# Kernel tuning notes

Hardware: AMD Instinct MI355X
Metric: run time of the kernel (lower is better)

Reference implementation:

```python
import jax, jax.numpy as jnp
import numpy as np

WS = 7          # window_size
NUM_HEADS = 8
EPS = 1e-5


def _layernorm(x, g, b):
    m = jnp.mean(x, axis=-1, keepdims=True)
    v = jnp.var(x, axis=-1, keepdims=True)
    return (x - m) * jax.lax.rsqrt(v + EPS) * g + b


def _window_attention(win, w_qkv, b_qkv, w_proj, b_proj):
    B_, L, C = win.shape
    h = NUM_HEADS
    d = C // h
    scale = d ** -0.5
    qkv = win @ w_qkv.T + b_qkv                      # (B_, L, 3C)
    qkv = qkv.reshape(B_, L, 3, h, d).transpose(2, 0, 3, 1, 4)  # (3, B_, h, L, d)
    q, k, v = qkv[0], qkv[1], qkv[2]
    attn = jnp.einsum('bhld,bhmd->bhlm', q, k) * scale
    attn = jax.nn.softmax(attn, axis=-1)
    out = jnp.einsum('bhlm,bhmd->bhld', attn, v)     # (B_, h, L, d)
    out = out.transpose(0, 2, 1, 3).reshape(B_, L, C)
    return out @ w_proj.T + b_proj


def _forward(x, H, W, g1, b1, w_qkv, b_qkv, w_proj, b_proj, g2, b2,
             w_fc1, b_fc1, w_fc2, b_fc2):
    N, L, C = x.shape
    shortcut = x
    y = _layernorm(x, g1, b1).reshape(N, H, W, C)
    pad_h = (WS - H % WS) % WS
    pad_w = (WS - W % WS) % WS
    y = jnp.pad(y, ((0, 0), (0, pad_h), (0, pad_w), (0, 0)))
    Hp, Wp = H + pad_h, W + pad_w
    # window partition: (N, Hp/WS, WS, Wp/WS, WS, C) -> (N*nW, WS*WS, C)
    y = y.reshape(N, Hp // WS, WS, Wp // WS, WS, C).transpose(0, 1, 3, 2, 4, 5)
    windows = y.reshape(-1, WS * WS, C)
    attn_windows = _window_attention(windows, w_qkv, b_qkv, w_proj, b_proj)
    # window reverse
    y = attn_windows.reshape(N, Hp // WS, Wp // WS, WS, WS, C)
    y = y.transpose(0, 1, 3, 2, 4, 5).reshape(N, Hp, Wp, C)[:, :H, :W, :]
    y = y.reshape(N, H * W, C)
    x = shortcut + y
    # MLP: Linear -> GELU (erf, torch default) -> Linear
    z = _layernorm(x, g2, b2)
    z = jax.nn.gelu(z @ w_fc1.T + b_fc1, approximate=False) @ w_fc2.T + b_fc2
    return x + z


def setup_inputs() -> dict:
    key = jax.random.key(0)
    ks = jax.random.split(key, 8)
    N, H, W, C = 8, 112, 112, 256
    hidden = 4 * C
    s = 0.02
    return {
        'x': jax.random.normal(ks[0], (N, H * W, C), jnp.float32),
        'H': H,
        'W': W,
        'g1': jnp.ones((C,), jnp.float32),
        'b1': jnp.zeros((C,), jnp.float32),
        'w_qkv': jax.random.normal(ks[1], (3 * C, C), jnp.float32) * s,
        'b_qkv': jnp.zeros((3 * C,), jnp.float32),
        'w_proj': jax.random.normal(ks[2], (C, C), jnp.float32) * s,
        'b_proj': jnp.zeros((C,), jnp.float32),
        'g2': jnp.ones((C,), jnp.float32),
        'b2': jnp.zeros((C,), jnp.float32),
        'w_fc1': jax.random.normal(ks[3], (hidden, C), jnp.float32) * s,
        'b_fc1': jnp.zeros((hidden,), jnp.float32),
        'w_fc2': jax.random.normal(ks[4], (C, hidden), jnp.float32) * s,
        'b_fc2': jnp.zeros((C,), jnp.float32),
    }


def reference(x, H, W, g1, b1, w_qkv, b_qkv, w_proj, b_proj, g2, b2,
              w_fc1, b_fc1, w_fc2, b_fc2):
    return _forward(x, H, W, g1, b1, w_qkv, b_qkv, w_proj, b_proj,
                    g2, b2, w_fc1, b_fc1, w_fc2, b_fc2)
```

## Files before the change

### kernel.cpp

```cpp
#include <hip/hip_runtime.h>
#include <hip/hip_bf16.h>
#include <cstdint>
#include <cstddef>


typedef __bf16 bf16x8 __attribute__((ext_vector_type(8)));
typedef float f32x4 __attribute__((ext_vector_type(4)));

__device__ __forceinline__ unsigned short f2bf(float f){
    union{float f;uint32_t u;}c;c.f=f;uint32_t u=c.u;u+=0x7fffu+((u>>16)&1u);return (unsigned short)(u>>16);}
__device__ __forceinline__ float gelu_f(float x){ return 0.5f*x*(1.0f+erff(x*0.70710678118654752f)); }
__device__ __forceinline__ int swz(int row,int g){ return (g & ~7) | ((g ^ row) & 7); }

__global__ __launch_bounds__(256) void conv_k(
    const float* __restrict__ src, unsigned short* __restrict__ dst, int n4)
{
    int i = blockIdx.x * 256 + threadIdx.x;
    if (i >= n4) return;
    float4 v = *(const float4*)(src + (size_t)i * 4);
    uint2 o;
    o.x = (uint32_t)f2bf(v.x) | ((uint32_t)f2bf(v.y) << 16);
    o.y = (uint32_t)f2bf(v.z) | ((uint32_t)f2bf(v.w) << 16);
    *(uint2*)(dst + (size_t)i * 4) = o;
}

__global__ __launch_bounds__(1024, 4) void attn_half_k(
    const float* __restrict__ x, const float* __restrict__ g1, const float* __restrict__ b1,
    const unsigned short* __restrict__ Wqkv, const float* __restrict__ bqkv,
    const unsigned short* __restrict__ Wproj, const float* __restrict__ bproj,
    float* __restrict__ out)
{
    __shared__ __align__(16) unsigned short yb[64 * 256];
    __shared__ __align__(16) unsigned short qkb[64 * 512];
    __shared__ __align__(16) unsigned short vtb[256 * 64];
    const int t = threadIdx.x, lane = t & 63, w = t >> 6;
    const int quad = lane >> 4, l16 = lane & 15;
    const int widx = blockIdx.x;
    const int img = widx >> 8, wi = widx & 255;
    const int wy = wi >> 4, wx = wi & 15;
    const size_t ibase = (size_t)img * 12544;

    for (int tok = w; tok < 49; tok += 16) {
        int r = tok / 7, c = tok - r * 7;
        size_t gtok = ibase + (size_t)(wy * 7 + r) * 112 + (wx * 7 + c);
        float4 v = *(const float4*)(x + gtok * 256 + lane * 4);
        float s = v.x + v.y + v.z + v.w;
        float q = v.x*v.x + v.y*v.y + v.z*v.z + v.w*v.w;
        #pragma unroll
        for (int o = 32; o > 0; o >>= 1) { s += __shfl_xor(s, o); q += __shfl_xor(q, o); }
        float mean = s * (1.f/256.f), var = q * (1.f/256.f) - mean * mean;
        float inv = rsqrtf(var + 1e-5f);
        float4 gv = *(const float4*)(g1 + lane * 4);
        float4 bv = *(const float4*)(b1 + lane * 4);
        uint2 pk;
        pk.x = (uint32_t)f2bf((v.x-mean)*inv*gv.x+bv.x) | ((uint32_t)f2bf((v.y-mean)*inv*gv.y+bv.y) << 16);
        pk.y = (uint32_t)f2bf((v.z-mean)*inv*gv.z+bv.z) | ((uint32_t)f2bf((v.w-mean)*inv*gv.w+bv.w) << 16);
        *(uint2*)&yb[tok*256 + swz(tok, lane >> 1)*8 + (lane & 1)*4] = pk;
    }
    {
        uint2 z2; z2.x = 0u; z2.y = 0u;
        for (int i = t; i < 960; i += 1024) {
            int row = 49 + (i >> 6), c4 = (i & 63) * 4;
            *(uint2*)&yb[row*256 + c4] = z2;
        }
    }
    __syncthreads();

    {
        const int n0 = w * 48;
        f32x4 acc[4][3] = {};
        #pragma unroll
        for (int ks = 0; ks < 8; ++ks) {
            bf16x8 af[4], bfr[3];
            #pragma unroll
            for (int mt = 0; mt < 4; ++mt) {
                int m = mt * 16 + l16;
                af[mt] = *(const bf16x8*)&yb[m*256 + swz(m, ks*4 + quad)*8];
            }
            #pragma unroll
            for (int nt = 0; nt < 3; ++nt) {
                int n = n0 + nt * 16 + l16;
                bfr[nt] = *(const bf16x8*)(Wqkv + (size_t)n*256 + ks*32 + quad*8);
            }
            #pragma unroll
            for (int mt = 0; mt < 4; ++mt)
                #pragma unroll
                for (int nt = 0; nt < 3; ++nt)
                    acc[mt][nt] = __builtin_amdgcn_mfma_f32_16x16x32_bf16(
                        af[mt], bfr[nt], acc[mt][nt], 0, 0, 0);
        }
        #pragma unroll
        for (int mt = 0; mt < 4; ++mt)
            #pragma unroll
            for (int nt = 0; nt < 3; ++nt) {
                int col = n0 + nt * 16 + l16;
                float bb = bqkv[col];
                #pragma unroll
                for (int r = 0; r < 4; ++r) {
                    int row = mt * 16 + quad * 4 + r;
                    unsigned short val = f2bf(acc[mt][nt][r] + bb);
                    if (col < 512)
                        qkb[row*512 + swz(row, col >> 3)*8 + (col & 7)] = val;
                    else
                        vtb[(col - 512)*64 + swz(col - 512, row >> 3)*8 + (row & 7)] = val;
                }
            }
    }
    __syncthreads();

    {
        const float scale = 0.17677669529663687f;
        const int h = w & 7, half = w >> 3;
        unsigned short* pbuf = qkb + w * 1280;

        bf16x8 aq[2], bk[4];
        #pragma unroll
        for (int mtl = 0; mtl < 2; ++mtl) {
            int m = half*32 + mtl*16 + l16;
            aq[mtl] = *(const bf16x8*)&qkb[m*512 + swz(m, h*4 + quad)*8];
        }
        #pragma unroll
        for (int nt = 0; nt < 4; ++nt) {
            int n = nt * 16 + l16;
            bk[nt] = *(const bf16x8*)&qkb[n*512 + swz(n, 32 + h*4 + quad)*8];
        }
        __syncthreads();

        f32x4 s[2][4] = {};
        #pragma unroll
        for (int mtl = 0; mtl < 2; ++mtl)
            #pragma unroll
            for (int nt = 0; nt < 4; ++nt)
                s[mtl][nt] = __builtin_amdgcn_mfma_f32_16x16x32_bf16(
                    aq[mtl], bk[nt], s[mtl][nt], 0, 0, 0);

        uint32_t pk01[2][4], pk23[2][4];
        #pragma unroll
        for (int mtl = 0; mtl < 2; ++mtl)
            #pragma unroll
            for (int r = 0; r < 4; ++r) {
                float v0 = s[mtl][0][r];
                float v1 = s[mtl][1][r];
                float v2 = s[mtl][2][r];
                float v3 = (l16 == 0) ? s[mtl][3][r] : -1e30f;
                float mxv = fmaxf(fmaxf(v0, v1), fmaxf(v2, v3));
                #pragma unroll
                for (int off = 8; off > 0; off >>= 1) mxv = fmaxf(mxv, __shfl_xor(mxv, off));
                float p0 = __expf((v0 - mxv) * scale);
                float p1 = __expf((v1 - mxv) * scale);
                float p2 = __expf((v2 - mxv) * scale);
                float p3 = __expf((v3 - mxv) * scale);
                float ssum = p0 + p1 + p2 + p3;
                #pragma unroll
                for (int off = 8; off > 0; off >>= 1) ssum += __shfl_xor(ssum, off);
                float inv = 1.f / ssum;
                pk01[mtl][r] = (uint32_t)f2bf(p0*inv) | ((uint32_t)f2bf(p1*inv) << 16);
                pk23[mtl][r] = (uint32_t)f2bf(p2*inv) | ((uint32_t)f2bf(p3*inv) << 16);
            }

        f32x4 o[2][2] = {};
        #pragma unroll
        for (int kst = 0; kst < 2; ++kst) {
            #pragma unroll
            for (int mtl = 0; mtl < 2; ++mtl)
                #pragma unroll
                for (int r = 0; r < 4; ++r) {
                    int lr = mtl*16 + quad*4 + r;
                    uint32_t pw = kst ? pk23[mtl][r] : pk01[mtl][r];
                    pbuf[lr*40 + l16]      = (unsigned short)(pw & 0xffffu);
                    pbuf[lr*40 + 16 + l16] = (unsigned short)(pw >> 16);
                }
            bf16x8 ap[2], bv[2];
            #pragma unroll
            for (int mtl = 0; mtl < 2; ++mtl) {
                int m = mtl * 16 + l16;
                ap[mtl] = *(const bf16x8*)&pbuf[m*40 + quad*8];
            }
            #pragma unroll
            for (int nt = 0; nt < 2; ++nt) {
                int c = h*32 + nt*16 + l16;
                bv[nt] = *(const bf16x8*)&vtb[c*64 + swz(c, kst*4 + quad)*8];
            }
            #pragma unroll
            for (int mtl = 0; mtl < 2; ++mtl)
                #pragma unroll
                for (int nt = 0; nt < 2; ++nt)
                    o[mtl][nt] = __builtin_amdgcn_mfma_f32_16x16x32_bf16(
                        ap[mtl], bv[nt], o[mtl][nt], 0, 0, 0);
        }
        __syncthreads();

        #pragma unroll
        for (int mtl = 0; mtl < 2; ++mtl)
            #pragma unroll
            for (int nt = 0; nt < 2; ++nt)
                #pragma unroll
                for (int r = 0; r < 4; ++r) {
                    int row = half*32 + mtl*16 + quad*4 + r;
                    int ch = h*32 + nt*16 + l16;
                    float val = (row < 49) ? o[mtl][nt][r] : 0.f;
                    qkb[row*512 + swz(row, ch >> 3)*8 + (ch & 7)] = f2bf(val);
                }
    }
    __syncthreads();

    {
        const int n0 = w * 16;
        f32x4 acc[4];
        #pragma unroll
        for (int mt = 0; mt < 4; ++mt) acc[mt] = (f32x4){0.f,0.f,0.f,0.f};
        #pragma unroll
        for (int ks = 0; ks < 8; ++ks) {
            bf16x8 af[4], bfr;
            #pragma unroll
            for (int mt = 0; mt < 4; ++mt) {
                int m = mt * 16 + l16;
                af[mt] = *(const bf16x8*)&qkb[m*512 + swz(m, ks*4 + quad)*8];
            }
            {
                int n = n0 + l16;
                bfr = *(const bf16x8*)(Wproj + (size_t)n*256 + ks*32 + quad*8);
            }
            #pragma unroll
            for (int mt = 0; mt < 4; ++mt)
                acc[mt] = __builtin_amdgcn_mfma_f32_16x16x32_bf16(
                    af[mt], bfr, acc[mt], 0, 0, 0);
        }
        #pragma unroll
        for (int mt = 0; mt < 4; ++mt)
            #pragma unroll
            for (int r = 0; r < 4; ++r) {
                int row = mt * 16 + quad * 4 + r;
                if (row < 49) {
                    int rr = row / 7, cc = row - rr * 7;
                    size_t gtok = ibase + (size_t)(wy * 7 + rr) * 112 + (wx * 7 + cc);
                    int col = n0 + l16;
                    out[gtok * 256 + col] = acc[mt][r] + bproj[col] + x[gtok * 256 + col];
                }
            }
    }
}

__global__ __launch_bounds__(512, 4) void mlp_half_k(
    const float* __restrict__ g2, const float* __restrict__ b2,
    const unsigned short* __restrict__ W1, const float* __restrict__ bf1,
    const unsigned short* __restrict__ W2, const float* __restrict__ bf2,
    float* __restrict__ out)
{
    __shared__ __align__(16) unsigned short zb[64 * 256];
    __shared__ __align__(16) unsigned short hb[64 * 256];
    const int t = threadIdx.x, lane = t & 63, w = t >> 6;
    const int quad = lane >> 4, l16 = lane & 15;
    const size_t m0 = (size_t)blockIdx.x * 64;

    for (int tok = w; tok < 64; tok += 8) {
        size_t row = m0 + tok;
        float4 v = *(const float4*)&out[row*256 + lane*4];
        float s = v.x+v.y+v.z+v.w, q = v.x*v.x+v.y*v.y+v.z*v.z+v.w*v.w;
        #pragma unroll
        for (int o = 32; o > 0; o >>= 1) { s += __shfl_xor(s, o); q += __shfl_xor(q, o); }
        float mean = s*(1.f/256.f), var = q*(1.f/256.f) - mean*mean;
        float inv = rsqrtf(var + 1e-5f);
        float4 gv = *(const float4*)(g2 + lane*4);
        float4 bv = *(const float4*)(b2 + lane*4);
        uint2 pk;
        pk.x = (uint32_t)f2bf((v.x-mean)*inv*gv.x+bv.x) | ((uint32_t)f2bf((v.y-mean)*inv*gv.y+bv.y) << 16);
        pk.y = (uint32_t)f2bf((v.z-mean)*inv*gv.z+bv.z) | ((uint32_t)f2bf((v.w-mean)*inv*gv.w+bv.w) << 16);
        *(uint2*)&zb[tok*256 + swz(tok, lane >> 1)*8 + (lane & 1)*4] = pk;
    }
    __syncthreads();

    f32x4 acc2[4][2] = {};
    for (int c = 0; c < 4; ++c) {
        const int hc0 = c * 256;
        f32x4 acc1[4][2] = {};
        #pragma unroll
        for (int ks = 0; ks < 8; ++ks) {
            bf16x8 af[4], bfr[2];
            #pragma unroll
            for (int mt = 0; mt < 4; ++mt) {
                int m = mt * 16 + l16;
                af[mt] = *(const bf16x8*)&zb[m*256 + swz(m, ks*4 + quad)*8];
            }
            #pragma unroll
            for (int nt = 0; nt < 2; ++nt) {
                int n = hc0 + w * 32 + nt * 16 + l16;
                bfr[nt] = *(const bf16x8*)(W1 + (size_t)n*256 + ks*32 + quad*8);
            }
            #pragma unroll
            for (int mt = 0; mt < 4; ++mt)
                #pragma unroll
                for (int nt = 0; nt < 2; ++nt)
                    acc1[mt][nt] = __builtin_amdgcn_mfma_f32_16x16x32_bf16(
                        af[mt], bfr[nt], acc1[mt][nt], 0, 0, 0);
        }
        __syncthreads();
        #pragma unroll
        for (int mt = 0; mt < 4; ++mt)
            #pragma unroll
            for (int nt = 0; nt < 2; ++nt) {
                int lc = w * 32 + nt * 16 + l16;
                float bb = bf1[hc0 + lc];
                #pragma unroll
                for (int r = 0; r < 4; ++r) {
                    int row = mt * 16 + quad * 4 + r;
                    hb[row*256 + swz(row, lc >> 3)*8 + (lc & 7)] =
                        f2bf(gelu_f(acc1[mt][nt][r] + bb));
                }
            }
        __syncthreads();
        #pragma unroll
        for (int ks = 0; ks < 8; ++ks) {
            bf16x8 af[4], bfr[2];
            #pragma unroll
            for (int mt = 0; mt < 4; ++mt) {
                int m = mt * 16 + l16;
                af[mt] = *(const bf16x8*)&hb[m*256 + swz(m, ks*4 + quad)*8];
            }
            #pragma unroll
            for (int nt = 0; nt < 2; ++nt) {
                int n = w * 32 + nt * 16 + l16;
                bfr[nt] = *(const bf16x8*)(W2 + (size_t)n*1024 + hc0 + ks*32 + quad*8);
            }
            #pragma unroll
            for (int mt = 0; mt < 4; ++mt)
                #pragma unroll
                for (int nt = 0; nt < 2; ++nt)
                    acc2[mt][nt] = __builtin_amdgcn_mfma_f32_16x16x32_bf16(
                        af[mt], bfr[nt], acc2[mt][nt], 0, 0, 0);
        }
    }
    #pragma unroll
    for (int mt = 0; mt < 4; ++mt)
        #pragma unroll
        for (int nt = 0; nt < 2; ++nt) {
            int col = w * 32 + nt * 16 + l16;
            float bb = bf2[col];
            #pragma unroll
            for (int r = 0; r < 4; ++r) {
                size_t row = m0 + mt * 16 + quad * 4 + r;
                out[row*256 + col] = acc2[mt][nt][r] + bb + out[row*256 + col];
            }
        }
}

extern "C" void kernel_launch(void* const* d_in, const int* in_sizes, int n_in,
                              void* d_out, int out_size, void* d_ws, size_t ws_size,
                              hipStream_t stream)
{
    const float* x      = (const float*)d_in[0];
    const float* g1     = (const float*)d_in[3];
    const float* b1     = (const float*)d_in[4];
    const float* w_qkv  = (const float*)d_in[5];
    const float* b_qkv  = (const float*)d_in[6];
    const float* w_proj = (const float*)d_in[7];
    const float* b_proj = (const float*)d_in[8];
    const float* g2     = (const float*)d_in[9];
    const float* b2     = (const float*)d_in[10];
    const float* w_fc1  = (const float*)d_in[11];
    const float* b_fc1  = (const float*)d_in[12];
    const float* w_fc2  = (const float*)d_in[13];
    const float* b_fc2  = (const float*)d_in[14];
    float* out = (float*)d_out;

    unsigned short* cWqkv  = (unsigned short*)d_ws;
    unsigned short* cWproj = cWqkv  + 196608;
    unsigned short* cWfc1  = cWproj + 65536;
    unsigned short* cWfc2  = cWfc1  + 262144;

    conv_k<<<192, 256, 0, stream>>>(w_qkv,  cWqkv,  49152);
    conv_k<<<64,  256, 0, stream>>>(w_proj, cWproj, 16384);
    conv_k<<<256, 256, 0, stream>>>(w_fc1,  cWfc1,  65536);
    conv_k<<<256, 256, 0, stream>>>(w_fc2,  cWfc2,  65536);

    attn_half_k<<<2048, 1024, 0, stream>>>(x, g1, b1, cWqkv, b_qkv, cWproj, b_proj, out);
    mlp_half_k<<<1568, 512, 0, stream>>>(g2, b2, cWfc1, b_fc1, cWfc2, b_fc2, out);
}
```

Baseline: 716.0 us.

## Stage epilogues through LDS for coalesced float4 stores and widen MLP block

Both kernels now write their GEMM outputs to shared memory and then do residual adds with coalesced float4 global loads and stores, replacing scattered scalar global writes. The MLP kernel doubles its threads to 1024 so each wave computes 16 columns instead of 32, and pads LDS row strides (QKP, MP, SP) to cut bank conflicts. LayerNorm token loads are batched into registers so several global loads are in flight before the reductions run. The changes add extra barriers and more LDS per block, and per-wave register pressure shifts.

```diff
diff --git a/kernel.cpp b/kernel.cpp
--- a/kernel.cpp
+++ b/kernel.cpp
@@ -24,6 +24,7 @@
     *(uint2*)(dst + (size_t)i * 4) = o;
 }
 
+#define QKP 520
 __global__ __launch_bounds__(1024, 4) void attn_half_k(
     const float* __restrict__ x, const float* __restrict__ g1, const float* __restrict__ b1,
     const unsigned short* __restrict__ Wqkv, const float* __restrict__ bqkv,
@@ -31,7 +32,7 @@
     float* __restrict__ out)
 {
     __shared__ __align__(16) unsigned short yb[64 * 256];
-    __shared__ __align__(16) unsigned short qkb[64 * 512];
+    __shared__ __align__(16) unsigned short qkb[64 * QKP];
     __shared__ __align__(16) unsigned short vtb[256 * 64];
     const int t = threadIdx.x, lane = t & 63, w = t >> 6;
     const int quad = lane >> 4, l16 = lane & 15;
@@ -40,22 +41,36 @@
     const int wy = wi >> 4, wx = wi & 15;
     const size_t ibase = (size_t)img * 12544;
 
-    for (int tok = w; tok < 49; tok += 16) {
-        int r = tok / 7, c = tok - r * 7;
-        size_t gtok = ibase + (size_t)(wy * 7 + r) * 112 + (wx * 7 + c);
-        float4 v = *(const float4*)(x + gtok * 256 + lane * 4);
-        float s = v.x + v.y + v.z + v.w;
-        float q = v.x*v.x + v.y*v.y + v.z*v.z + v.w*v.w;
-        #pragma unroll
-        for (int o = 32; o > 0; o >>= 1) { s += __shfl_xor(s, o); q += __shfl_xor(q, o); }
-        float mean = s * (1.f/256.f), var = q * (1.f/256.f) - mean * mean;
-        float inv = rsqrtf(var + 1e-5f);
+    {
+        float4 xv[4];
+        #pragma unroll
+        for (int i = 0; i < 4; ++i) {
+            int tok = w + i * 16;
+            if (tok < 49) {
+                int r = tok / 7, c = tok - r * 7;
+                size_t gtok = ibase + (size_t)(wy * 7 + r) * 112 + (wx * 7 + c);
+                xv[i] = *(const float4*)(x + gtok * 256 + lane * 4);
+            }
+        }
         float4 gv = *(const float4*)(g1 + lane * 4);
         float4 bv = *(const float4*)(b1 + lane * 4);
-        uint2 pk;
-        pk.x = (uint32_t)f2bf((v.x-mean)*inv*gv.x+bv.x) | ((uint32_t)f2bf((v.y-mean)*inv*gv.y+bv.y) << 16);
-        pk.y = (uint32_t)f2bf((v.z-mean)*inv*gv.z+bv.z) | ((uint32_t)f2bf((v.w-mean)*inv*gv.w+bv.w) << 16);
-        *(uint2*)&yb[tok*256 + swz(tok, lane >> 1)*8 + (lane & 1)*4] = pk;
+        #pragma unroll
+        for (int i = 0; i < 4; ++i) {
+            int tok = w + i * 16;
+            if (tok < 49) {
+                float4 v = xv[i];
+                float s = v.x + v.y + v.z + v.w;
+                float q = v.x*v.x + v.y*v.y + v.z*v.z + v.w*v.w;
+                #pragma unroll
+                for (int o = 32; o > 0; o >>= 1) { s += __shfl_xor(s, o); q += __shfl_xor(q, o); }
+                float mean = s * (1.f/256.f), var = q * (1.f/256.f) - mean * mean;
+                float inv = rsqrtf(var + 1e-5f);
+                uint2 pk;
+                pk.x = (uint32_t)f2bf((v.x-mean)*inv*gv.x+bv.x) | ((uint32_t)f2bf((v.y-mean)*inv*gv.y+bv.y) << 16);
+                pk.y = (uint32_t)f2bf((v.z-mean)*inv*gv.z+bv.z) | ((uint32_t)f2bf((v.w-mean)*inv*gv.w+bv.w) << 16);
+                *(uint2*)&yb[tok*256 + swz(tok, lane >> 1)*8 + (lane & 1)*4] = pk;
+            }
+        }
     }
     {
         uint2 z2; z2.x = 0u; z2.y = 0u;
@@ -100,7 +115,7 @@
                     int row = mt * 16 + quad * 4 + r;
                     unsigned short val = f2bf(acc[mt][nt][r] + bb);
                     if (col < 512)
-                        qkb[row*512 + swz(row, col >> 3)*8 + (col & 7)] = val;
+                        qkb[row*QKP + swz(row, col >> 3)*8 + (col & 7)] = val;
                     else
                         vtb[(col - 512)*64 + swz(col - 512, row >> 3)*8 + (row & 7)] = val;
                 }
@@ -117,12 +132,12 @@
         #pragma unroll
         for (int mtl = 0; mtl < 2; ++mtl) {
             int m = half*32 + mtl*16 + l16;
-            aq[mtl] = *(const bf16x8*)&qkb[m*512 + swz(m, h*4 + quad)*8];
+            aq[mtl] = *(const bf16x8*)&qkb[m*QKP + swz(m, h*4 + quad)*8];
         }
         #pragma unroll
         for (int nt = 0; nt < 4; ++nt) {
             int n = nt * 16 + l16;
-            bk[nt] = *(const bf16x8*)&qkb[n*512 + swz(n, 32 + h*4 + quad)*8];
+            bk[nt] = *(const bf16x8*)&qkb[n*QKP + swz(n, 32 + h*4 + quad)*8];
         }
         __syncthreads();
 
@@ -199,7 +214,7 @@
                     int row = half*32 + mtl*16 + quad*4 + r;
                     int ch = h*32 + nt*16 + l16;
                     float val = (row < 49) ? o[mtl][nt][r] : 0.f;
-                    qkb[row*512 + swz(row, ch >> 3)*8 + (ch & 7)] = f2bf(val);
+                    qkb[row*QKP + swz(row, ch >> 3)*8 + (ch & 7)] = f2bf(val);
                 }
     }
     __syncthreads();
@@ -215,7 +230,7 @@
             #pragma unroll
             for (int mt = 0; mt < 4; ++mt) {
                 int m = mt * 16 + l16;
-                af[mt] = *(const bf16x8*)&qkb[m*512 + swz(m, ks*4 + quad)*8];
+                af[mt] = *(const bf16x8*)&qkb[m*QKP + swz(m, ks*4 + quad)*8];
             }
             {
                 int n = n0 + l16;
@@ -226,122 +241,158 @@
                 acc[mt] = __builtin_amdgcn_mfma_f32_16x16x32_bf16(
                     af[mt], bfr, acc[mt], 0, 0, 0);
         }
-        #pragma unroll
-        for (int mt = 0; mt < 4; ++mt)
-            #pragma unroll
-            for (int r = 0; r < 4; ++r) {
-                int row = mt * 16 + quad * 4 + r;
+        float* sb = (float*)yb;
+        float4 bp = *(const float4*)(bproj + lane * 4);
+        #pragma unroll
+        for (int batch = 0; batch < 2; ++batch) {
+            #pragma unroll
+            for (int mt = 2*batch; mt < 2*batch + 2; ++mt)
+                #pragma unroll
+                for (int r = 0; r < 4; ++r) {
+                    int row = mt * 16 + quad * 4 + r;
+                    sb[(row - batch*32)*256 + n0 + l16] = acc[mt][r];
+                }
+            __syncthreads();
+            #pragma unroll
+            for (int i = 0; i < 2; ++i) {
+                int row = batch*32 + w*2 + i;
                 if (row < 49) {
                     int rr = row / 7, cc = row - rr * 7;
                     size_t gtok = ibase + (size_t)(wy * 7 + rr) * 112 + (wx * 7 + cc);
-                    int col = n0 + l16;
-                    out[gtok * 256 + col] = acc[mt][r] + bproj[col] + x[gtok * 256 + col];
-                }
-            }
+                    float4 xr = *(const float4*)(x + gtok * 256 + lane * 4);
+                    float4 sv = *(const float4*)&sb[(row - batch*32)*256 + lane * 4];
+                    float4 o4;
+                    o4.x = sv.x + bp.x + xr.x;
+                    o4.y = sv.y + bp.y + xr.y;
+                    o4.z = sv.z + bp.z + xr.z;
+                    o4.w = sv.w + bp.w + xr.w;
+                    *(float4*)&out[gtok * 256 + lane * 4] = o4;
+                }
+            }
+            __syncthreads();
+        }
     }
 }
 
-__global__ __launch_bounds__(512, 4) void mlp_half_k(
+#define MP 264
+#define SP 260
+__global__ __launch_bounds__(1024, 8) void mlp_half_k(
     const float* __restrict__ g2, const float* __restrict__ b2,
     const unsigned short* __restrict__ W1, const float* __restrict__ bf1,
     const unsigned short* __restrict__ W2, const float* __restrict__ bf2,
     float* __restrict__ out)
 {
-    __shared__ __align__(16) unsigned short zb[64 * 256];
-    __shared__ __align__(16) unsigned short hb[64 * 256];
+    __shared__ __align__(16) unsigned short smem[2 * 64 * MP];
+    unsigned short* zb = smem;
+    unsigned short* hb = smem + 64 * MP;
     const int t = threadIdx.x, lane = t & 63, w = t >> 6;
     const int quad = lane >> 4, l16 = lane & 15;
     const size_t m0 = (size_t)blockIdx.x * 64;
 
-    for (int tok = w; tok < 64; tok += 8) {
-        size_t row = m0 + tok;
-        float4 v = *(const float4*)&out[row*256 + lane*4];
-        float s = v.x+v.y+v.z+v.w, q = v.x*v.x+v.y*v.y+v.z*v.z+v.w*v.w;
-        #pragma unroll
-        for (int o = 32; o > 0; o >>= 1) { s += __shfl_xor(s, o); q += __shfl_xor(q, o); }
-        float mean = s*(1.f/256.f), var = q*(1.f/256.f) - mean*mean;
-        float inv = rsqrtf(var + 1e-5f);
+    {
+        float4 xv[4];
+        #pragma unroll
+        for (int i = 0; i < 4; ++i) {
+            size_t row = m0 + w + i * 16;
+            xv[i] = *(const float4*)&out[row*256 + lane*4];
+        }
         float4 gv = *(const float4*)(g2 + lane*4);
         float4 bv = *(const float4*)(b2 + lane*4);
-        uint2 pk;
-        pk.x = (uint32_t)f2bf((v.x-mean)*inv*gv.x+bv.x) | ((uint32_t)f2bf((v.y-mean)*inv*gv.y+bv.y) << 16);
-        pk.y = (uint32_t)f2bf((v.z-mean)*inv*gv.z+bv.z) | ((uint32_t)f2bf((v.w-mean)*inv*gv.w+bv.w) << 16);
-        *(uint2*)&zb[tok*256 + swz(tok, lane >> 1)*8 + (lane & 1)*4] = pk;
+        #pragma unroll
+        for (int i = 0; i < 4; ++i) {
+            int tok = w + i * 16;
+            float4 v = xv[i];
+            float s = v.x+v.y+v.z+v.w, q = v.x*v.x+v.y*v.y+v.z*v.z+v.w*v.w;
+            #pragma unroll
+            for (int o = 32; o > 0; o >>= 1) { s += __shfl_xor(s, o); q += __shfl_xor(q, o); }
+            float mean = s*(1.f/256.f), var = q*(1.f/256.f) - mean*mean;
+            float inv = rsqrtf(var + 1e-5f);
+            uint2 pk;
+            pk.x = (uint32_t)f2bf((v.x-mean)*inv*gv.x+bv.x) | ((uint32_t)f2bf((v.y-mean)*inv*gv.y+bv.y) << 16);
+            pk.y = (uint32_t)f2bf((v.z-mean)*inv*gv.z+bv.z) | ((uint32_t)f2bf((v.w-mean)*inv*gv.w+bv.w) << 16);
+            *(uint2*)&zb[tok*MP + swz(tok, lane >> 1)*8 + (lane & 1)*4] = pk;
+        }
     }
     __syncthreads();
 
-    f32x4 acc2[4][2] = {};
+    f32x4 acc2[4] = {};
     for (int c = 0; c < 4; ++c) {
         const int hc0 = c * 256;
-        f32x4 acc1[4][2] = {};
+        f32x4 acc1[4] = {};
         #pragma unroll
         for (int ks = 0; ks < 8; ++ks) {
-            bf16x8 af[4], bfr[2];
+            bf16x8 af[4], bfr;
             #pragma unroll
             for (int mt = 0; mt < 4; ++mt) {
                 int m = mt * 16 + l16;
-                af[mt] = *(const bf16x8*)&zb[m*256 + swz(m, ks*4 + quad)*8];
-            }
-            #pragma unroll
-            for (int nt = 0; nt < 2; ++nt) {
-                int n = hc0 + w * 32 + nt * 16 + l16;
-                bfr[nt] = *(const bf16x8*)(W1 + (size_t)n*256 + ks*32 + quad*8);
+                af[mt] = *(const bf16x8*)&zb[m*MP + swz(m, ks*4 + quad)*8];
+            }
+            {
+                int n = hc0 + w * 16 + l16;
+                bfr = *(const bf16x8*)(W1 + (size_t)n*256 + ks*32 + quad*8);
             }
             #pragma unroll
             for (int mt = 0; mt < 4; ++mt)
-                #pragma unroll
-                for (int nt = 0; nt < 2; ++nt)
-                    acc1[mt][nt] = __builtin_amdgcn_mfma_f32_16x16x32_bf16(
-                        af[mt], bfr[nt], acc1[mt][nt], 0, 0, 0);
+                acc1[mt] = __builtin_amdgcn_mfma_f32_16x16x32_bf16(
+                    af[mt], bfr, acc1[mt], 0, 0, 0);
         }
         __syncthreads();
-        #pragma unroll
-        for (int mt = 0; mt < 4; ++mt)
-            #pragma unroll
-            for (int nt = 0; nt < 2; ++nt) {
-                int lc = w * 32 + nt * 16 + l16;
-                float bb = bf1[hc0 + lc];
+        {
+            int lc = w * 16 + l16;
+            float bb = bf1[hc0 + lc];
+            #pragma unroll
+            for (int mt = 0; mt < 4; ++mt)
                 #pragma unroll
                 for (int r = 0; r < 4; ++r) {
                     int row = mt * 16 + quad * 4 + r;
-                    hb[row*256 + swz(row, lc >> 3)*8 + (lc & 7)] =
-                        f2bf(gelu_f(acc1[mt][nt][r] + bb));
-                }
-            }
+                    hb[row*MP + swz(row, lc >> 3)*8 + (lc & 7)] =
+                        f2bf(gelu_f(acc1[mt][r] + bb));
+                }
+        }
         __syncthreads();
         #pragma unroll
         for (int ks = 0; ks < 8; ++ks) {
-            bf16x8 af[4], bfr[2];
+            bf16x8 af[4], bfr;
             #pragma unroll
             for (int mt = 0; mt < 4; ++mt) {
                 int m = mt * 16 + l16;
-                af[mt] = *(const bf16x8*)&hb[m*256 + swz(m, ks*4 + quad)*8];
-            }
-            #pragma unroll
-            for (int nt = 0; nt < 2; ++nt) {
-                int n = w * 32 + nt * 16 + l16;
-                bfr[nt] = *(const bf16x8*)(W2 + (size_t)n*1024 + hc0 + ks*32 + quad*8);
+                af[mt] = *(const bf16x8*)&hb[m*MP + swz(m, ks*4 + quad)*8];
+            }
+            {
+                int n = w * 16 + l16;
+                bfr = *(const bf16x8*)(W2 + (size_t)n*1024 + hc0 + ks*32 + quad*8);
             }
             #pragma unroll
             for (int mt = 0; mt < 4; ++mt)
-                #pragma unroll
-                for (int nt = 0; nt < 2; ++nt)
-                    acc2[mt][nt] = __builtin_amdgcn_mfma_f32_16x16x32_bf16(
-                        af[mt], bfr[nt], acc2[mt][nt], 0, 0, 0);
-        }
-    }
-    #pragma unroll
-    for (int mt = 0; mt < 4; ++mt)
-        #pragma unroll
-        for (int nt = 0; nt < 2; ++nt) {
-            int col = w * 32 + nt * 16 + l16;
-            float bb = bf2[col];
+                acc2[mt] = __builtin_amdgcn_mfma_f32_16x16x32_bf16(
+                    af[mt], bfr, acc2[mt], 0, 0, 0);
+        }
+    }
+    __syncthreads();
+    {
+        float* sbuf = (float*)smem;
+        int col = w * 16 + l16;
+        float bb = bf2[col];
+        #pragma unroll
+        for (int mt = 0; mt < 4; ++mt)
             #pragma unroll
             for (int r = 0; r < 4; ++r) {
-                size_t row = m0 + mt * 16 + quad * 4 + r;
-                out[row*256 + col] = acc2[mt][nt][r] + bb + out[row*256 + col];
-            }
-        }
+                int row = mt * 16 + quad * 4 + r;
+                sbuf[row*SP + col] = acc2[mt][r] + bb;
+            }
+        __syncthreads();
+        #pragma unroll
+        for (int i = 0; i < 4; ++i) {
+            int row = w * 4 + i;
+            size_t g = (m0 + row) * 256 + lane * 4;
+            float4 rv = *(const float4*)&out[g];
+            float4 sv = *(const float4*)&sbuf[row*SP + lane*4];
+            float4 o4;
+            o4.x = rv.x + sv.x; o4.y = rv.y + sv.y;
+            o4.z = rv.z + sv.z; o4.w = rv.w + sv.w;
+            *(float4*)&out[g] = o4;
+        }
+    }
 }
 
 extern "C" void kernel_launch(void* const* d_in, const int* in_sizes, int n_in,
@@ -374,5 +425,5 @@
     conv_k<<<256, 256, 0, stream>>>(w_fc2,  cWfc2,  65536);
 
     attn_half_k<<<2048, 1024, 0, stream>>>(x, g1, b1, cWqkv, b_qkv, cWproj, b_proj, out);
-    mlp_half_k<<<1568, 512, 0, stream>>>(g2, b2, cWfc1, b_fc1, cWfc2, b_fc2, out);
+    mlp_half_k<<<1568, 1024, 0, stream>>>(g2, b2, cWfc1, b_fc1, cWfc2, b_fc2, out);
 }
```

Measured after the change: 775.7 us. 8.3% more time.

## Batch loads, prefetch weight fragments, and vectorize epilogue stores in both kernels

Applied to the files above, without the earlier changes.

The attention kernel now issues all of a wave's token loads before its LayerNorm reductions. Its projection epilogue stages accumulators through shared memory so that the residual read and output write become coalesced float4 accesses. The MLP kernel remaps columns so each lane owns an adjacent pair, which allows packed 32-bit GELU writes to LDS and float2 residual updates. It also double-buffers the W1/W2 fragment loads one k-step ahead to hide global latency. The costs are extra barriers and LDS traffic in the attention epilogue and higher register pressure from the prefetch buffers.

```diff
diff --git a/kernel.cpp b/kernel.cpp
--- a/kernel.cpp
+++ b/kernel.cpp
@@ -40,22 +40,36 @@
     const int wy = wi >> 4, wx = wi & 15;
     const size_t ibase = (size_t)img * 12544;
 
-    for (int tok = w; tok < 49; tok += 16) {
-        int r = tok / 7, c = tok - r * 7;
-        size_t gtok = ibase + (size_t)(wy * 7 + r) * 112 + (wx * 7 + c);
-        float4 v = *(const float4*)(x + gtok * 256 + lane * 4);
-        float s = v.x + v.y + v.z + v.w;
-        float q = v.x*v.x + v.y*v.y + v.z*v.z + v.w*v.w;
-        #pragma unroll
-        for (int o = 32; o > 0; o >>= 1) { s += __shfl_xor(s, o); q += __shfl_xor(q, o); }
-        float mean = s * (1.f/256.f), var = q * (1.f/256.f) - mean * mean;
-        float inv = rsqrtf(var + 1e-5f);
+    {
+        float4 xv[4];
+        #pragma unroll
+        for (int i = 0; i < 4; ++i) {
+            int tok = w + i * 16;
+            if (tok < 49) {
+                int r = tok / 7, c = tok - r * 7;
+                size_t gtok = ibase + (size_t)(wy * 7 + r) * 112 + (wx * 7 + c);
+                xv[i] = *(const float4*)(x + gtok * 256 + lane * 4);
+            }
+        }
         float4 gv = *(const float4*)(g1 + lane * 4);
         float4 bv = *(const float4*)(b1 + lane * 4);
-        uint2 pk;
-        pk.x = (uint32_t)f2bf((v.x-mean)*inv*gv.x+bv.x) | ((uint32_t)f2bf((v.y-mean)*inv*gv.y+bv.y) << 16);
-        pk.y = (uint32_t)f2bf((v.z-mean)*inv*gv.z+bv.z) | ((uint32_t)f2bf((v.w-mean)*inv*gv.w+bv.w) << 16);
-        *(uint2*)&yb[tok*256 + swz(tok, lane >> 1)*8 + (lane & 1)*4] = pk;
+        #pragma unroll
+        for (int i = 0; i < 4; ++i) {
+            int tok = w + i * 16;
+            if (tok < 49) {
+                float4 v = xv[i];
+                float s = v.x + v.y + v.z + v.w;
+                float q = v.x*v.x + v.y*v.y + v.z*v.z + v.w*v.w;
+                #pragma unroll
+                for (int o = 32; o > 0; o >>= 1) { s += __shfl_xor(s, o); q += __shfl_xor(q, o); }
+                float mean = s * (1.f/256.f), var = q * (1.f/256.f) - mean * mean;
+                float inv = rsqrtf(var + 1e-5f);
+                uint2 pk;
+                pk.x = (uint32_t)f2bf((v.x-mean)*inv*gv.x+bv.x) | ((uint32_t)f2bf((v.y-mean)*inv*gv.y+bv.y) << 16);
+                pk.y = (uint32_t)f2bf((v.z-mean)*inv*gv.z+bv.z) | ((uint32_t)f2bf((v.w-mean)*inv*gv.w+bv.w) << 16);
+                *(uint2*)&yb[tok*256 + swz(tok, lane >> 1)*8 + (lane & 1)*4] = pk;
+            }
+        }
     }
     {
         uint2 z2; z2.x = 0u; z2.y = 0u;
@@ -226,18 +240,36 @@
                 acc[mt] = __builtin_amdgcn_mfma_f32_16x16x32_bf16(
                     af[mt], bfr, acc[mt], 0, 0, 0);
         }
-        #pragma unroll
-        for (int mt = 0; mt < 4; ++mt)
-            #pragma unroll
-            for (int r = 0; r < 4; ++r) {
-                int row = mt * 16 + quad * 4 + r;
+        float* sb = (float*)yb;
+        float4 bp = *(const float4*)(bproj + lane * 4);
+        #pragma unroll
+        for (int batch = 0; batch < 2; ++batch) {
+            #pragma unroll
+            for (int mt = 2*batch; mt < 2*batch + 2; ++mt)
+                #pragma unroll
+                for (int r = 0; r < 4; ++r) {
+                    int row = mt * 16 + quad * 4 + r;
+                    sb[(row - batch*32)*256 + n0 + l16] = acc[mt][r];
+                }
+            __syncthreads();
+            #pragma unroll
+            for (int i = 0; i < 2; ++i) {
+                int row = batch*32 + w*2 + i;
                 if (row < 49) {
                     int rr = row / 7, cc = row - rr * 7;
                     size_t gtok = ibase + (size_t)(wy * 7 + rr) * 112 + (wx * 7 + cc);
-                    int col = n0 + l16;
-                    out[gtok * 256 + col] = acc[mt][r] + bproj[col] + x[gtok * 256 + col];
-                }
-            }
+                    float4 xr = *(const float4*)(x + gtok * 256 + lane * 4);
+                    float4 sv = *(const float4*)&sb[(row - batch*32)*256 + lane * 4];
+                    float4 o4;
+                    o4.x = sv.x + bp.x + xr.x;
+                    o4.y = sv.y + bp.y + xr.y;
+                    o4.z = sv.z + bp.z + xr.z;
+                    o4.w = sv.w + bp.w + xr.w;
+                    *(float4*)&out[gtok * 256 + lane * 4] = o4;
+                }
+            }
+            __syncthreads();
+        }
     }
 }
 
@@ -252,6 +284,7 @@
     const int t = threadIdx.x, lane = t & 63, w = t >> 6;
     const int quad = lane >> 4, l16 = lane & 15;
     const size_t m0 = (size_t)blockIdx.x * 64;
+    const int cpair = w * 32 + 2 * l16;
 
     for (int tok = w; tok < 64; tok += 8) {
         size_t row = m0 + tok;
@@ -274,74 +307,95 @@
     for (int c = 0; c < 4; ++c) {
         const int hc0 = c * 256;
         f32x4 acc1[4][2] = {};
+        bf16x8 bnx[2];
+        #pragma unroll
+        for (int nt = 0; nt < 2; ++nt) {
+            int n = hc0 + cpair + nt;
+            bnx[nt] = *(const bf16x8*)(W1 + (size_t)n*256 + quad*8);
+        }
         #pragma unroll
         for (int ks = 0; ks < 8; ++ks) {
-            bf16x8 af[4], bfr[2];
+            bf16x8 af[4], bcur[2];
+            bcur[0] = bnx[0]; bcur[1] = bnx[1];
+            if (ks < 7) {
+                #pragma unroll
+                for (int nt = 0; nt < 2; ++nt) {
+                    int n = hc0 + cpair + nt;
+                    bnx[nt] = *(const bf16x8*)(W1 + (size_t)n*256 + (ks+1)*32 + quad*8);
+                }
+            }
             #pragma unroll
             for (int mt = 0; mt < 4; ++mt) {
                 int m = mt * 16 + l16;
                 af[mt] = *(const bf16x8*)&zb[m*256 + swz(m, ks*4 + quad)*8];
             }
             #pragma unroll
-            for (int nt = 0; nt < 2; ++nt) {
-                int n = hc0 + w * 32 + nt * 16 + l16;
-                bfr[nt] = *(const bf16x8*)(W1 + (size_t)n*256 + ks*32 + quad*8);
-            }
-            #pragma unroll
             for (int mt = 0; mt < 4; ++mt)
                 #pragma unroll
                 for (int nt = 0; nt < 2; ++nt)
                     acc1[mt][nt] = __builtin_amdgcn_mfma_f32_16x16x32_bf16(
-                        af[mt], bfr[nt], acc1[mt][nt], 0, 0, 0);
+                        af[mt], bcur[nt], acc1[mt][nt], 0, 0, 0);
         }
         __syncthreads();
-        #pragma unroll
-        for (int mt = 0; mt < 4; ++mt)
-            #pragma unroll
-            for (int nt = 0; nt < 2; ++nt) {
-                int lc = w * 32 + nt * 16 + l16;
-                float bb = bf1[hc0 + lc];
+        {
+            float bb0 = bf1[hc0 + cpair];
+            float bb1 = bf1[hc0 + cpair + 1];
+            #pragma unroll
+            for (int mt = 0; mt < 4; ++mt)
                 #pragma unroll
                 for (int r = 0; r < 4; ++r) {
                     int row = mt * 16 + quad * 4 + r;
-                    hb[row*256 + swz(row, lc >> 3)*8 + (lc & 7)] =
-                        f2bf(gelu_f(acc1[mt][nt][r] + bb));
-                }
-            }
+                    uint32_t pk = (uint32_t)f2bf(gelu_f(acc1[mt][0][r] + bb0))
+                                | ((uint32_t)f2bf(gelu_f(acc1[mt][1][r] + bb1)) << 16);
+                    *(uint32_t*)&hb[row*256 + swz(row, cpair >> 3)*8 + (cpair & 7)] = pk;
+                }
+        }
         __syncthreads();
+        bf16x8 b2x[2];
+        #pragma unroll
+        for (int nt = 0; nt < 2; ++nt) {
+            int n = cpair + nt;
+            b2x[nt] = *(const bf16x8*)(W2 + (size_t)n*1024 + hc0 + quad*8);
+        }
         #pragma unroll
         for (int ks = 0; ks < 8; ++ks) {
-            bf16x8 af[4], bfr[2];
+            bf16x8 af[4], bcur[2];
+            bcur[0] = b2x[0]; bcur[1] = b2x[1];
+            if (ks < 7) {
+                #pragma unroll
+                for (int nt = 0; nt < 2; ++nt) {
+                    int n = cpair + nt;
+                    b2x[nt] = *(const bf16x8*)(W2 + (size_t)n*1024 + hc0 + (ks+1)*32 + quad*8);
+                }
+            }
             #pragma unroll
             for (int mt = 0; mt < 4; ++mt) {
                 int m = mt * 16 + l16;
                 af[mt] = *(const bf16x8*)&hb[m*256 + swz(m, ks*4 + quad)*8];
             }
             #pragma unroll
-            for (int nt = 0; nt < 2; ++nt) {
-                int n = w * 32 + nt * 16 + l16;
-                bfr[nt] = *(const bf16x8*)(W2 + (size_t)n*1024 + hc0 + ks*32 + quad*8);
-            }
-            #pragma unroll
             for (int mt = 0; mt < 4; ++mt)
                 #pragma unroll
                 for (int nt = 0; nt < 2; ++nt)
                     acc2[mt][nt] = __builtin_amdgcn_mfma_f32_16x16x32_bf16(
-                        af[mt], bfr[nt], acc2[mt][nt], 0, 0, 0);
-        }
-    }
-    #pragma unroll
-    for (int mt = 0; mt < 4; ++mt)
-        #pragma unroll
-        for (int nt = 0; nt < 2; ++nt) {
-            int col = w * 32 + nt * 16 + l16;
-            float bb = bf2[col];
+                        af[mt], bcur[nt], acc2[mt][nt], 0, 0, 0);
+        }
+    }
+    {
+        float bb0 = bf2[cpair];
+        float bb1 = bf2[cpair + 1];
+        #pragma unroll
+        for (int mt = 0; mt < 4; ++mt)
             #pragma unroll
             for (int r = 0; r < 4; ++r) {
                 size_t row = m0 + mt * 16 + quad * 4 + r;
-                out[row*256 + col] = acc2[mt][nt][r] + bb + out[row*256 + col];
-            }
-        }
+                float2 rv = *(const float2*)&out[row*256 + cpair];
+                float2 o2;
+                o2.x = acc2[mt][0][r] + bb0 + rv.x;
+                o2.y = acc2[mt][1][r] + bb1 + rv.y;
+                *(float2*)&out[row*256 + cpair] = o2;
+            }
+    }
 }
 
 extern "C" void kernel_launch(void* const* d_in, const int* in_sizes, int n_in,
```

Result: faster. 683.4 us (-4.6%).

## Fuse window attention and MLP into one per-window kernel

Applied to the files above, without the earlier changes.

Merges the attention kernel and the MLP kernel into a single kernel that processes each 7x7 window end-to-end. The residual and post-projection activations stay in shared memory (reusing the qkv buffer) instead of being written to and re-read from global memory, and the second layernorm is computed in-block. The MLP now runs on 64-row tiles where only 49 rows are valid, so about a quarter of its MFMA work is padding. LDS buffers are reused across stages, one barrier is dropped, and weight loads are software-prefetched one k-step ahead.

```diff
diff --git a/kernel.cpp b/kernel.cpp
--- a/kernel.cpp
+++ b/kernel.cpp
@@ -24,10 +24,13 @@
     *(uint2*)(dst + (size_t)i * 4) = o;
 }
 
-__global__ __launch_bounds__(1024, 4) void attn_half_k(
+__global__ __launch_bounds__(1024, 4) void fused_k(
     const float* __restrict__ x, const float* __restrict__ g1, const float* __restrict__ b1,
     const unsigned short* __restrict__ Wqkv, const float* __restrict__ bqkv,
     const unsigned short* __restrict__ Wproj, const float* __restrict__ bproj,
+    const float* __restrict__ g2, const float* __restrict__ b2,
+    const unsigned short* __restrict__ W1, const float* __restrict__ bf1,
+    const unsigned short* __restrict__ W2, const float* __restrict__ bf2,
     float* __restrict__ out)
 {
     __shared__ __align__(16) unsigned short yb[64 * 256];
@@ -39,23 +42,38 @@
     const int img = widx >> 8, wi = widx & 255;
     const int wy = wi >> 4, wx = wi & 15;
     const size_t ibase = (size_t)img * 12544;
-
-    for (int tok = w; tok < 49; tok += 16) {
-        int r = tok / 7, c = tok - r * 7;
-        size_t gtok = ibase + (size_t)(wy * 7 + r) * 112 + (wx * 7 + c);
-        float4 v = *(const float4*)(x + gtok * 256 + lane * 4);
-        float s = v.x + v.y + v.z + v.w;
-        float q = v.x*v.x + v.y*v.y + v.z*v.z + v.w*v.w;
-        #pragma unroll
-        for (int o = 32; o > 0; o >>= 1) { s += __shfl_xor(s, o); q += __shfl_xor(q, o); }
-        float mean = s * (1.f/256.f), var = q * (1.f/256.f) - mean * mean;
-        float inv = rsqrtf(var + 1e-5f);
+    float* res = (float*)qkb;
+
+    {
+        float4 xv[4];
+        #pragma unroll
+        for (int i = 0; i < 4; ++i) {
+            int tok = w + i * 16;
+            if (tok < 49) {
+                int r = tok / 7, c = tok - r * 7;
+                size_t gtok = ibase + (size_t)(wy * 7 + r) * 112 + (wx * 7 + c);
+                xv[i] = *(const float4*)(x + gtok * 256 + lane * 4);
+            }
+        }
         float4 gv = *(const float4*)(g1 + lane * 4);
         float4 bv = *(const float4*)(b1 + lane * 4);
-        uint2 pk;
-        pk.x = (uint32_t)f2bf((v.x-mean)*inv*gv.x+bv.x) | ((uint32_t)f2bf((v.y-mean)*inv*gv.y+bv.y) << 16);
-        pk.y = (uint32_t)f2bf((v.z-mean)*inv*gv.z+bv.z) | ((uint32_t)f2bf((v.w-mean)*inv*gv.w+bv.w) << 16);
-        *(uint2*)&yb[tok*256 + swz(tok, lane >> 1)*8 + (lane & 1)*4] = pk;
+        #pragma unroll
+        for (int i = 0; i < 4; ++i) {
+            int tok = w + i * 16;
+            if (tok < 49) {
+                float4 v = xv[i];
+                float s = v.x + v.y + v.z + v.w;
+                float q = v.x*v.x + v.y*v.y + v.z*v.z + v.w*v.w;
+                #pragma unroll
+                for (int o = 32; o > 0; o >>= 1) { s += __shfl_xor(s, o); q += __shfl_xor(q, o); }
+                float mean = s * (1.f/256.f), var = q * (1.f/256.f) - mean * mean;
+                float inv = rsqrtf(var + 1e-5f);
+                uint2 pk;
+                pk.x = (uint32_t)f2bf((v.x-mean)*inv*gv.x+bv.x) | ((uint32_t)f2bf((v.y-mean)*inv*gv.y+bv.y) << 16);
+                pk.y = (uint32_t)f2bf((v.z-mean)*inv*gv.z+bv.z) | ((uint32_t)f2bf((v.w-mean)*inv*gv.w+bv.w) << 16);
+                *(uint2*)&yb[tok*256 + swz(tok, lane >> 1)*8 + (lane & 1)*4] = pk;
+            }
+        }
     }
     {
         uint2 z2; z2.x = 0u; z2.y = 0u;
@@ -188,8 +206,6 @@
                     o[mtl][nt] = __builtin_amdgcn_mfma_f32_16x16x32_bf16(
                         ap[mtl], bv[nt], o[mtl][nt], 0, 0, 0);
         }
-        __syncthreads();
-
         #pragma unroll
         for (int mtl = 0; mtl < 2; ++mtl)
             #pragma unroll
@@ -199,7 +215,7 @@
                     int row = half*32 + mtl*16 + quad*4 + r;
                     int ch = h*32 + nt*16 + l16;
                     float val = (row < 49) ? o[mtl][nt][r] : 0.f;
-                    qkb[row*512 + swz(row, ch >> 3)*8 + (ch & 7)] = f2bf(val);
+                    yb[row*256 + swz(row, ch >> 3)*8 + (ch & 7)] = f2bf(val);
                 }
     }
     __syncthreads();
@@ -215,7 +231,7 @@
             #pragma unroll
             for (int mt = 0; mt < 4; ++mt) {
                 int m = mt * 16 + l16;
-                af[mt] = *(const bf16x8*)&qkb[m*512 + swz(m, ks*4 + quad)*8];
+                af[mt] = *(const bf16x8*)&yb[m*256 + swz(m, ks*4 + quad)*8];
             }
             {
                 int n = n0 + l16;
@@ -226,6 +242,119 @@
                 acc[mt] = __builtin_amdgcn_mfma_f32_16x16x32_bf16(
                     af[mt], bfr, acc[mt], 0, 0, 0);
         }
+        float bb = bproj[n0 + l16];
+        #pragma unroll
+        for (int mt = 0; mt < 4; ++mt)
+            #pragma unroll
+            for (int r = 0; r < 4; ++r) {
+                int row = mt * 16 + quad * 4 + r;
+                res[row*256 + n0 + l16] = acc[mt][r] + bb;
+            }
+    }
+    __syncthreads();
+
+    {
+        const int row = t >> 4, i = t & 15;
+        float4 v0, v1, v2, v3;
+        v0 = *(const float4*)&res[row*256 + i*4];
+        v1 = *(const float4*)&res[row*256 + i*4 + 64];
+        v2 = *(const float4*)&res[row*256 + i*4 + 128];
+        v3 = *(const float4*)&res[row*256 + i*4 + 192];
+        if (row < 49) {
+            int rr = row / 7, cc = row - rr * 7;
+            size_t gtok = ibase + (size_t)(wy * 7 + rr) * 112 + (wx * 7 + cc);
+            const float* xr = x + gtok * 256;
+            float4 a0 = *(const float4*)(xr + i*4);
+            float4 a1 = *(const float4*)(xr + i*4 + 64);
+            float4 a2 = *(const float4*)(xr + i*4 + 128);
+            float4 a3 = *(const float4*)(xr + i*4 + 192);
+            v0.x+=a0.x; v0.y+=a0.y; v0.z+=a0.z; v0.w+=a0.w;
+            v1.x+=a1.x; v1.y+=a1.y; v1.z+=a1.z; v1.w+=a1.w;
+            v2.x+=a2.x; v2.y+=a2.y; v2.z+=a2.z; v2.w+=a2.w;
+            v3.x+=a3.x; v3.y+=a3.y; v3.z+=a3.z; v3.w+=a3.w;
+            *(float4*)&res[row*256 + i*4]       = v0;
+            *(float4*)&res[row*256 + i*4 + 64]  = v1;
+            *(float4*)&res[row*256 + i*4 + 128] = v2;
+            *(float4*)&res[row*256 + i*4 + 192] = v3;
+        }
+        float s = v0.x+v0.y+v0.z+v0.w + v1.x+v1.y+v1.z+v1.w
+                + v2.x+v2.y+v2.z+v2.w + v3.x+v3.y+v3.z+v3.w;
+        float q = v0.x*v0.x+v0.y*v0.y+v0.z*v0.z+v0.w*v0.w
+                + v1.x*v1.x+v1.y*v1.y+v1.z*v1.z+v1.w*v1.w
+                + v2.x*v2.x+v2.y*v2.y+v2.z*v2.z+v2.w*v2.w
+                + v3.x*v3.x+v3.y*v3.y+v3.z*v3.z+v3.w*v3.w;
+        #pragma unroll
+        for (int off = 8; off > 0; off >>= 1) { s += __shfl_xor(s, off); q += __shfl_xor(q, off); }
+        float mean = s * (1.f/256.f), var = q * (1.f/256.f) - mean * mean;
+        float inv = rsqrtf(var + 1e-5f);
+        #pragma unroll
+        for (int j = 0; j < 4; ++j) {
+            int c = i*4 + j*64;
+            float4 vv = (j==0)?v0:(j==1)?v1:(j==2)?v2:v3;
+            float4 gv = *(const float4*)(g2 + c);
+            float4 bv = *(const float4*)(b2 + c);
+            uint2 pk;
+            pk.x = (uint32_t)f2bf((vv.x-mean)*inv*gv.x+bv.x) | ((uint32_t)f2bf((vv.y-mean)*inv*gv.y+bv.y) << 16);
+            pk.y = (uint32_t)f2bf((vv.z-mean)*inv*gv.z+bv.z) | ((uint32_t)f2bf((vv.w-mean)*inv*gv.w+bv.w) << 16);
+            *(uint2*)&yb[row*256 + swz(row, c >> 3)*8 + (c & 7)] = pk;
+        }
+    }
+    __syncthreads();
+
+    unsigned short* hb = vtb;
+    f32x4 acc2[4] = {};
+    const int ncol = w * 16 + l16;
+    for (int c = 0; c < 4; ++c) {
+        const int hc0 = c * 256;
+        f32x4 acc1[4] = {};
+        bf16x8 bnx = *(const bf16x8*)(W1 + (size_t)(hc0 + ncol)*256 + quad*8);
+        #pragma unroll
+        for (int ks = 0; ks < 8; ++ks) {
+            bf16x8 af[4], bcur = bnx;
+            if (ks < 7)
+                bnx = *(const bf16x8*)(W1 + (size_t)(hc0 + ncol)*256 + (ks+1)*32 + quad*8);
+            #pragma unroll
+            for (int mt = 0; mt < 4; ++mt) {
+                int m = mt * 16 + l16;
+                af[mt] = *(const bf16x8*)&yb[m*256 + swz(m, ks*4 + quad)*8];
+            }
+            #pragma unroll
+            for (int mt = 0; mt < 4; ++mt)
+                acc1[mt] = __builtin_amdgcn_mfma_f32_16x16x32_bf16(
+                    af[mt], bcur, acc1[mt], 0, 0, 0);
+        }
+        __syncthreads();
+        {
+            float bb = bf1[hc0 + ncol];
+            #pragma unroll
+            for (int mt = 0; mt < 4; ++mt)
+                #pragma unroll
+                for (int r = 0; r < 4; ++r) {
+                    int row = mt * 16 + quad * 4 + r;
+                    hb[row*256 + swz(row, ncol >> 3)*8 + (ncol & 7)] =
+                        f2bf(gelu_f(acc1[mt][r] + bb));
+                }
+        }
+        __syncthreads();
+        bf16x8 b2x = *(const bf16x8*)(W2 + (size_t)ncol*1024 + hc0 + quad*8);
+        #pragma unroll
+        for (int ks = 0; ks < 8; ++ks) {
+            bf16x8 af[4], bcur = b2x;
+            if (ks < 7)
+                b2x = *(const bf16x8*)(W2 + (size_t)ncol*1024 + hc0 + (ks+1)*32 + quad*8);
+            #pragma unroll
+            for (int mt = 0; mt < 4; ++mt) {
+                int m = mt * 16 + l16;
+                af[mt] = *(const bf16x8*)&hb[m*256 + swz(m, ks*4 + quad)*8];
+            }
+            #pragma unroll
+            for (int mt = 0; mt < 4; ++mt)
+                acc2[mt] = __builtin_amdgcn_mfma_f32_16x16x32_bf16(
+                    af[mt], bcur, acc2[mt], 0, 0, 0);
+        }
+    }
+    {
+        float bb = bf2[ncol];
         #pragma unroll
         for (int mt = 0; mt < 4; ++mt)
             #pragma unroll
@@ -234,114 +363,10 @@
                 if (row < 49) {
                     int rr = row / 7, cc = row - rr * 7;
                     size_t gtok = ibase + (size_t)(wy * 7 + rr) * 112 + (wx * 7 + cc);
-                    int col = n0 + l16;
-                    out[gtok * 256 + col] = acc[mt][r] + bproj[col] + x[gtok * 256 + col];
+                    out[gtok * 256 + ncol] = acc2[mt][r] + bb + res[row*256 + ncol];
                 }
             }
     }
-}
-
-__global__ __launch_bounds__(512, 4) void mlp_half_k(
-    const float* __restrict__ g2, const float* __restrict__ b2,
-    const unsigned short* __restrict__ W1, const float* __restrict__ bf1,
-    const unsigned short* __restrict__ W2, const float* __restrict__ bf2,
-    float* __restrict__ out)
-{
-    __shared__ __align__(16) unsigned short zb[64 * 256];
-    __shared__ __align__(16) unsigned short hb[64 * 256];
-    const int t = threadIdx.x, lane = t & 63, w = t >> 6;
-    const int quad = lane >> 4, l16 = lane & 15;
-    const size_t m0 = (size_t)blockIdx.x * 64;
-
-    for (int tok = w; tok < 64; tok += 8) {
-        size_t row = m0 + tok;
-        float4 v = *(const float4*)&out[row*256 + lane*4];
-        float s = v.x+v.y+v.z+v.w, q = v.x*v.x+v.y*v.y+v.z*v.z+v.w*v.w;
-        #pragma unroll
-        for (int o = 32; o > 0; o >>= 1) { s += __shfl_xor(s, o); q += __shfl_xor(q, o); }
-        float mean = s*(1.f/256.f), var = q*(1.f/256.f) - mean*mean;
-        float inv = rsqrtf(var + 1e-5f);
-        float4 gv = *(const float4*)(g2 + lane*4);
-        float4 bv = *(const float4*)(b2 + lane*4);
-        uint2 pk;
-        pk.x = (uint32_t)f2bf((v.x-mean)*inv*gv.x+bv.x) | ((uint32_t)f2bf((v.y-mean)*inv*gv.y+bv.y) << 16);
-        pk.y = (uint32_t)f2bf((v.z-mean)*inv*gv.z+bv.z) | ((uint32_t)f2bf((v.w-mean)*inv*gv.w+bv.w) << 16);
-        *(uint2*)&zb[tok*256 + swz(tok, lane >> 1)*8 + (lane & 1)*4] = pk;
-    }
-    __syncthreads();
-
-    f32x4 acc2[4][2] = {};
-    for (int c = 0; c < 4; ++c) {
-        const int hc0 = c * 256;
-        f32x4 acc1[4][2] = {};
-        #pragma unroll
-        for (int ks = 0; ks < 8; ++ks) {
-            bf16x8 af[4], bfr[2];
-            #pragma unroll
-            for (int mt = 0; mt < 4; ++mt) {
-                int m = mt * 16 + l16;
-                af[mt] = *(const bf16x8*)&zb[m*256 + swz(m, ks*4 + quad)*8];
-            }
-            #pragma unroll
-            for (int nt = 0; nt < 2; ++nt) {
-                int n = hc0 + w * 32 + nt * 16 + l16;
-                bfr[nt] = *(const bf16x8*)(W1 + (size_t)n*256 + ks*32 + quad*8);
-            }
-            #pragma unroll
-            for (int mt = 0; mt < 4; ++mt)
-                #pragma unroll
-                for (int nt = 0; nt < 2; ++nt)
-                    acc1[mt][nt] = __builtin_amdgcn_mfma_f32_16x16x32_bf16(
-                        af[mt], bfr[nt], acc1[mt][nt], 0, 0, 0);
-        }
-        __syncthreads();
-        #pragma unroll
-        for (int mt = 0; mt < 4; ++mt)
-            #pragma unroll
-            for (int nt = 0; nt < 2; ++nt) {
-                int lc = w * 32 + nt * 16 + l16;
-                float bb = bf1[hc0 + lc];
-                #pragma unroll
-                for (int r = 0; r < 4; ++r) {
-                    int row = mt * 16 + quad * 4 + r;
-                    hb[row*256 + swz(row, lc >> 3)*8 + (lc & 7)] =
-                        f2bf(gelu_f(acc1[mt][nt][r] + bb));
-                }
-            }
-        __syncthreads();
-        #pragma unroll
-        for (int ks = 0; ks < 8; ++ks) {
-            bf16x8 af[4], bfr[2];
-            #pragma unroll
-            for (int mt = 0; mt < 4; ++mt) {
-                int m = mt * 16 + l16;
-                af[mt] = *(const bf16x8*)&hb[m*256 + swz(m, ks*4 + quad)*8];
-            }
-            #pragma unroll
-            for (int nt = 0; nt < 2; ++nt) {
-                int n = w * 32 + nt * 16 + l16;
-                bfr[nt] = *(const bf16x8*)(W2 + (size_t)n*1024 + hc0 + ks*32 + quad*8);
-            }
-            #pragma unroll
-            for (int mt = 0; mt < 4; ++mt)
-                #pragma unroll
-                for (int nt = 0; nt < 2; ++nt)
-                    acc2[mt][nt] = __builtin_amdgcn_mfma_f32_16x16x32_bf16(
-                        af[mt], bfr[nt], acc2[mt][nt], 0, 0, 0);
-        }
-    }
-    #pragma unroll
-    for (int mt = 0; mt < 4; ++mt)
-        #pragma unroll
-        for (int nt = 0; nt < 2; ++nt) {
-            int col = w * 32 + nt * 16 + l16;
-            float bb = bf2[col];
-            #pragma unroll
-            for (int r = 0; r < 4; ++r) {
-                size_t row = m0 + mt * 16 + quad * 4 + r;
-                out[row*256 + col] = acc2[mt][nt][r] + bb + out[row*256 + col];
-            }
-        }
 }
 
 extern "C" void kernel_launch(void* const* d_in, const int* in_sizes, int n_in,
@@ -373,6 +398,6 @@
     conv_k<<<256, 256, 0, stream>>>(w_fc1,  cWfc1,  65536);
     conv_k<<<256, 256, 0, stream>>>(w_fc2,  cWfc2,  65536);
 
-    attn_half_k<<<2048, 1024, 0, stream>>>(x, g1, b1, cWqkv, b_qkv, cWproj, b_proj, out);
-    mlp_half_k<<<1568, 512, 0, stream>>>(g2, b2, cWfc1, b_fc1, cWfc2, b_fc2, out);
+    fused_k<<<2048, 1024, 0, stream>>>(x, g1, b1, cWqkv, b_qkv, cWproj, b_proj,
+                                       g2, b2, cWfc1, b_fc1, cWfc2, b_fc2, out);
 }
```

Result: faster. 697.4 us (-2.6%).
